# Kernel tuning notes

Hardware: AMD Instinct MI355X
Metric: run time of the kernel (lower is better)

Reference implementation:

```python
import jax, jax.numpy as jnp
import numpy as np

N = 20000       # nodes
E = 320000      # edges (before self-loops)
F_IN = 1024     # num_features
H = 4           # head_num
C = 64          # hidden_size
NC = 4          # n_classes
NEG_SLOPE = 0.2 # PyG GATConv default


def setup_inputs() -> dict:
    key = jax.random.key(0)
    ks = jax.random.split(key, 16)
    def w(k, shape, fan_in):
        return jax.random.normal(k, shape, dtype=jnp.float32) / np.sqrt(fan_in)
    x = jax.random.normal(ks[0], (N, F_IN), dtype=jnp.float32)
    edge_index = jax.random.randint(ks[1], (2, E), 0, N, dtype=jnp.int64)
    return {
        "x": x,
        "edge_index": edge_index,
        # layer 1: F_IN -> H*C, concat
        "w1": w(ks[2], (F_IN, H * C), F_IN),
        "as1": w(ks[3], (H, C), C),
        "ad1": w(ks[4], (H, C), C),
        "b1": jnp.zeros((H * C,), jnp.float32),
        # layer 2: H*C -> H*C, concat
        "w2": w(ks[5], (H * C, H * C), H * C),
        "as2": w(ks[6], (H, C), C),
        "ad2": w(ks[7], (H, C), C),
        "b2": jnp.zeros((H * C,), jnp.float32),
        # out layer: H*C -> C, 1 head, concat=False
        "w3": w(ks[8], (H * C, 1 * C), H * C),
        "as3": w(ks[9], (1, C), C),
        "ad3": w(ks[10], (1, C), C),
        "b3": jnp.zeros((C,), jnp.float32),
        # classifier
        "wc": w(ks[11], (C, NC), C),
        "bc": jnp.zeros((NC,), jnp.float32),
    }


def gat_layer(x, src, dst, W, a_src, a_dst, bias, concat):
    """PyG GATConv (eval mode, self-loops already added to src/dst)."""
    n = x.shape[0]
    Hh, Cc = a_src.shape
    h = (x @ W).reshape(n, Hh, Cc)                       # [N,H,C]
    al_s = jnp.sum(h * a_src[None], axis=-1)             # [N,H]
    al_d = jnp.sum(h * a_dst[None], axis=-1)             # [N,H]
    e = al_s[src] + al_d[dst]                            # [E,H]
    e = jax.nn.leaky_relu(e, NEG_SLOPE)
    # segment softmax over incoming edges of each destination node
    emax = jax.ops.segment_max(e, dst, num_segments=n)   # [N,H]
    ex = jnp.exp(e - emax[dst])
    denom = jax.ops.segment_sum(ex, dst, num_segments=n) # [N,H]
    alpha = ex / (denom[dst] + 1e-16)                    # [E,H]
    msg = h[src] * alpha[..., None]                      # [E,H,C]
    out = jax.ops.segment_sum(msg, dst, num_segments=n)  # [N,H,C]
    if concat:
        out = out.reshape(n, Hh * Cc)
    else:
        out = out.mean(axis=1)
    return out + bias


def reference(x, edge_index, w1, as1, ad1, b1, w2, as2, ad2, b2,
              w3, as3, ad3, b3, wc, bc):
    n = x.shape[0]
    loop = jnp.arange(n, dtype=edge_index.dtype)
    src = jnp.concatenate([edge_index[0], loop])
    dst = jnp.concatenate([edge_index[1], loop])
    out = jax.nn.relu(gat_layer(x, src, dst, w1, as1, ad1, b1, True))
    out = jax.nn.relu(gat_layer(out, src, dst, w2, as2, ad2, b2, True))
    out = gat_layer(out, src, dst, w3, as3, ad3, b3, False)
    return out @ wc + bc                                  # [N, n_classes]
```

## Files before the change

### kernel.cpp

```cpp
#include <hip/hip_runtime.h>

#define N_NODES 20000
#define N_EDGES 320000
#define ET (N_EDGES + N_NODES)
#define F_IN 1024
#define HC 256
#define NC 4

typedef unsigned short ushort_t;
typedef __attribute__((ext_vector_type(8))) short short8;
typedef __attribute__((ext_vector_type(4))) float f32x4;

__device__ inline ushort_t f2bf(float f) {
    unsigned u = __float_as_uint(f);
    unsigned r = (u + 0x7fffu + ((u >> 16) & 1u)) >> 16;
    return (ushort_t)r;
}
__device__ inline float bf2f(ushort_t u) {
    return __uint_as_float(((unsigned)u) << 16);
}

__device__ inline unsigned cvt_pk_bf16(float lo, float hi) {
    unsigned r;
    asm("v_cvt_pk_bf16_f32 %0, %1, %2" : "=v"(r) : "v"(lo), "v"(hi));
    return r;
}

#define GLOAD16(gp, lp) __builtin_amdgcn_global_load_lds( \
    (const __attribute__((address_space(1))) void*)(gp),  \
    (__attribute__((address_space(3))) void*)(lp), 16, 0, 0)

__global__ void count_kernel(const int* __restrict__ ei, int* __restrict__ counts) {
    int e = blockIdx.x * blockDim.x + threadIdx.x;
    if (e >= ET) return;
    int dst = (e < N_EDGES) ? ei[N_EDGES + e] : (e - N_EDGES);
    atomicAdd(&counts[dst], 1);
}

__global__ void scan_kernel(const int* __restrict__ counts, int* __restrict__ row_ptr,
                            int* __restrict__ cursor) {
    __shared__ int sums[1024];
    int t = threadIdx.x;
    const int per = (N_NODES + 1023) / 1024;
    int b = t * per;
    int e = min(b + per, N_NODES);
    int s = 0;
    for (int i = b; i < e; ++i) s += counts[i];
    sums[t] = s;
    __syncthreads();
    for (int off = 1; off < 1024; off <<= 1) {
        int v = (t >= off) ? sums[t - off] : 0;
        __syncthreads();
        sums[t] += v;
        __syncthreads();
    }
    int run = (t == 0) ? 0 : sums[t - 1];
    for (int i = b; i < e; ++i) {
        row_ptr[i] = run;
        cursor[i]  = run;
        run += counts[i];
    }
    if (t == 0) row_ptr[N_NODES] = ET;
}

__global__ void scatter_kernel(const int* __restrict__ ei, int* __restrict__ cursor,
                               int* __restrict__ col) {
    int e = blockIdx.x * blockDim.x + threadIdx.x;
    if (e >= ET) return;
    int src, dst;
    if (e < N_EDGES) { src = ei[e]; dst = ei[N_EDGES + e]; }
    else             { src = dst = e - N_EDGES; }
    int pos = atomicAdd(&cursor[dst], 1);
    col[pos] = src;
}

__global__ void split_T(const float* __restrict__ in, ushort_t* __restrict__ hi,
                        ushort_t* __restrict__ lo, int K, int Nn) {
    int idx = blockIdx.x * blockDim.x + threadIdx.x;
    if (idx >= K * Nn) return;
    int k = idx / Nn, n = idx - k * Nn;
    float v = in[idx];
    ushort_t h = f2bf(v);
    hi[(size_t)n * K + k] = h;
    lo[(size_t)n * K + k] = f2bf(v - bf2f(h));
}

#define AL_EPILOGUE()                                                              \
    {                                                                              \
        float asv[NF], adv[NF];                                                    \
        _Pragma("unroll")                                                          \
        for (int j = 0; j < NF; ++j) {                                             \
            int col = bn + wn * SN + j * 16 + (lane & 15);                         \
            asv[j] = as_w[col];                                                    \
            adv[j] = ad_w[col];                                                    \
        }                                                                          \
        float* s_as = (float*)smem;                                   \
        float* s_ad = (float*)smem + 2 * BM;                                       \
        _Pragma("unroll")                                                          \
        for (int i = 0; i < MF; ++i) {                                             \
            _Pragma("unroll")                                                      \
            for (int rr = 0; rr < 4; ++rr) {                                       \
                float ps = 0.f, pd = 0.f;                                          \
                _Pragma("unroll")                                                  \
                for (int j = 0; j < NF; ++j) {                                     \
                    ps += acc[i][j][rr] * asv[j];                                  \
                    pd += acc[i][j][rr] * adv[j];                                  \
                }                                                                  \
                _Pragma("unroll")                                                  \
                for (int o = 1; o < 16; o <<= 1) {                                 \
                    ps += __shfl_xor(ps, o, 64);                                   \
                    pd += __shfl_xor(pd, o, 64);                                   \
                }                                                                  \
                if ((lane & 15) == 0) {                                            \
                    int rl = wm * SM + i * 16 + (lane >> 4) * 4 + rr;              \
                    s_as[wn * BM + rl] = ps;                                       \
                    s_ad[wn * BM + rl] = pd;                                       \
                }                                                                  \
            }                                                                      \
        }                                                                          \
        __syncthreads();                                                           \
        if (t < BM) {                                                              \
            int row = bm + t;                                                      \
            if (row < M) {                                                         \
                int hb = bn >> 6;                                                  \
                als[row * H + hb] = s_as[t] + s_as[BM + t];                        \
                ald[row * H + hb] = s_ad[t] + s_ad[BM + t];                        \
            }                                                                      \
        }                                                                          \
    }

template<int GY, int H>
__launch_bounds__(256)
__global__ void gemm_f32a(const float* __restrict__ X,
                          const ushort_t* __restrict__ BTh, const ushort_t* __restrict__ BTl,
                          float* __restrict__ C, const float* __restrict__ as_w,
                          const float* __restrict__ ad_w, float* __restrict__ als,
                          float* __restrict__ ald, int M, int K, int NT) {
    constexpr int BM = 128, BN = 64, SM = 64, SN = 32, MF = 4, NF = 2;
    __shared__ __align__(16) char smem[49152];

    const int t = threadIdx.x, lane = t & 63, w = t >> 6;
    const int wm = w >> 1, wn = w & 1;
    const int nwg = gridDim.x;
    const int id = blockIdx.x;
    const int q = nwg >> 3, r = nwg & 7;
    const int xcd = id & 7, idx = id >> 3;
    const int logical = (xcd < r ? xcd * (q + 1) : r * (q + 1) + (xcd - r) * q) + idx;
    const int bm = (logical / GY) * BM, bn = (logical % GY) * BN;

    const int achk = lane & 3;
    const float* xRow[2]; int aoff[2];
    #pragma unroll
    for (int qq = 0; qq < 2; ++qq) {
        int arow = (w * 2 + qq) * 16 + (lane >> 2);
        int grow = min(bm + arow, M - 1);
        xRow[qq] = X + (size_t)grow * K + achk * 8;
        aoff[qq] = arow * 64 + ((achk ^ ((arow >> 1) & 3)) * 16);
    }
    const int gchunk = ((lane & 3) ^ ((lane >> 3) & 3)) * 16;
    const int brow = w * 16 + (lane >> 2);
    const size_t gB = (size_t)(bn + brow) * K * 2 + gchunk;
    const int lB = w * 1024;

    const char* Bhb = (const char*)BTh;
    const char* Blb = (const char*)BTl;
    const int c16 = (lane >> 4);
    const int NTs = K / 64;

    f32x4 acc[MF][NF];
    #pragma unroll
    for (int i = 0; i < MF; ++i)
        #pragma unroll
        for (int j = 0; j < NF; ++j) acc[i][j] = (f32x4){0.f, 0.f, 0.f, 0.f};

    float4 cur0[2][2], cur1[2][2], nxt0[2][2], nxt1[2][2];
    #pragma unroll
    for (int qq = 0; qq < 2; ++qq)
        #pragma unroll
        for (int kc = 0; kc < 2; ++kc) {
            cur0[qq][kc] = *(const float4*)(xRow[qq] + kc * 32);
            cur1[qq][kc] = *(const float4*)(xRow[qq] + kc * 32 + 4);
        }

    for (int ts = 0; ts < NTs; ++ts) {
        size_t kb = (size_t)ts * 128;
        #pragma unroll
        for (int kc = 0; kc < 2; ++kc) {
            GLOAD16(Bhb + gB + kb + kc * 64, smem + 32768 + kc * 4096 + lB);
            GLOAD16(Blb + gB + kb + kc * 64, smem + 40960 + kc * 4096 + lB);
        }
        if (ts + 1 < NTs) {
            #pragma unroll
            for (int qq = 0; qq < 2; ++qq)
                #pragma unroll
                for (int kc = 0; kc < 2; ++kc) {
                    nxt0[qq][kc] = *(const float4*)(xRow[qq] + (ts + 1) * 64 + kc * 32);
                    nxt1[qq][kc] = *(const float4*)(xRow[qq] + (ts + 1) * 64 + kc * 32 + 4);
                }
        }
        #pragma unroll
        for (int qq = 0; qq < 2; ++qq)
            #pragma unroll
            for (int kc = 0; kc < 2; ++kc) {
                float vv[8] = {cur0[qq][kc].x, cur0[qq][kc].y, cur0[qq][kc].z, cur0[qq][kc].w,
                               cur1[qq][kc].x, cur1[qq][kc].y, cur1[qq][kc].z, cur1[qq][kc].w};
                unsigned hp[4], lp[4];
                #pragma unroll
                for (int j = 0; j < 4; ++j) {
                    unsigned h = cvt_pk_bf16(vv[2 * j], vv[2 * j + 1]);
                    float h0 = __uint_as_float(h << 16);
                    float h1 = __uint_as_float(h & 0xFFFF0000u);
                    hp[j] = h;
                    lp[j] = cvt_pk_bf16(vv[2 * j] - h0, vv[2 * j + 1] - h1);
                }
                *(uint4*)(smem + kc * 8192 + aoff[qq])         = make_uint4(hp[0], hp[1], hp[2], hp[3]);
                *(uint4*)(smem + 16384 + kc * 8192 + aoff[qq]) = make_uint4(lp[0], lp[1], lp[2], lp[3]);
            }
        __syncthreads();
        #pragma unroll
        for (int kc = 0; kc < 2; ++kc) {
            short8 afh[MF], afl[MF], bfh[NF], bfl[NF];
            #pragma unroll
            for (int i = 0; i < MF; ++i) {
                int row = wm * SM + i * 16 + (lane & 15);
                int off = row * 64 + ((c16 ^ ((row >> 1) & 3)) * 16);
                afh[i] = *(const short8*)(smem + kc * 8192 + off);
                afl[i] = *(const short8*)(smem + 16384 + kc * 8192 + off);
            }
            #pragma unroll
            for (int j = 0; j < NF; ++j) {
                int row = wn * SN + j * 16 + (lane & 15);
                int off = row * 64 + ((c16 ^ ((row >> 1) & 3)) * 16);
                bfh[j] = *(const short8*)(smem + 32768 + kc * 4096 + off);
                bfl[j] = *(const short8*)(smem + 40960 + kc * 4096 + off);
            }
            #pragma unroll
            for (int i = 0; i < MF; ++i)
                #pragma unroll
                for (int j = 0; j < NF; ++j) {
                    acc[i][j] = __builtin_amdgcn_mfma_f32_16x16x32_bf16(afh[i], bfh[j], acc[i][j], 0, 0, 0);
                    acc[i][j] = __builtin_amdgcn_mfma_f32_16x16x32_bf16(afh[i], bfl[j], acc[i][j], 0, 0, 0);
                    acc[i][j] = __builtin_amdgcn_mfma_f32_16x16x32_bf16(afl[i], bfh[j], acc[i][j], 0, 0, 0);
                }
        }
        __syncthreads();
        #pragma unroll
        for (int qq = 0; qq < 2; ++qq)
            #pragma unroll
            for (int kc = 0; kc < 2; ++kc) { cur0[qq][kc] = nxt0[qq][kc]; cur1[qq][kc] = nxt1[qq][kc]; }
    }
    #pragma unroll
    for (int i = 0; i < MF; ++i) {
        int rbase = bm + wm * SM + i * 16 + (lane >> 4) * 4;
        #pragma unroll
        for (int j = 0; j < NF; ++j) {
            int col = bn + wn * SN + j * 16 + (lane & 15);
            #pragma unroll
            for (int rr = 0; rr < 4; ++rr)
                if (rbase + rr < M) C[(size_t)(rbase + rr) * NT + col] = acc[i][j][rr];
        }
    }
    AL_EPILOGUE()
}

template<int BMT, int GY, int H>
__launch_bounds__(256)
__global__ void gemm_mfma(const ushort_t* __restrict__ Ah, const ushort_t* __restrict__ Al,
                          const ushort_t* __restrict__ BTh, const ushort_t* __restrict__ BTl,
                          float* __restrict__ C, const float* __restrict__ as_w,
                          const float* __restrict__ ad_w, float* __restrict__ als,
                          float* __restrict__ ald, int M, int K, int NT) {
    constexpr int BM = BMT, BN = 64, SM = BM / 2, SN = 32, MF = SM / 16, NF = 2;
    constexpr int AQ = BM / 64;
    constexpr int ASZ = BM * 64;
    __shared__ __align__(16) char smem[4 * ASZ + 16384];

    const int t = threadIdx.x, lane = t & 63, w = t >> 6;
    const int wm = w >> 1, wn = w & 1;
    const int nwg = gridDim.x;
    const int id = blockIdx.x;
    const int q = nwg >> 3, r = nwg & 7;
    const int xcd = id & 7, idx = id >> 3;
    const int logical = (xcd < r ? xcd * (q + 1) : r * (q + 1) + (xcd - r) * q) + idx;
    const int bm = (logical / GY) * BM, bn = (logical % GY) * BN;
    const int gchunk = ((lane & 3) ^ ((lane >> 3) & 3)) * 16;

    size_t gA[AQ]; int lA[AQ];
    #pragma unroll
    for (int qq = 0; qq < AQ; ++qq) {
        int inst = w * AQ + qq;
        int arow = inst * 16 + (lane >> 2);
        int grow = min(bm + arow, M - 1);
        gA[qq] = (size_t)grow * K * 2 + gchunk;
        lA[qq] = inst * 1024;
    }
    const int brow = w * 16 + (lane >> 2);
    const size_t gB = (size_t)(bn + brow) * K * 2 + gchunk;
    const int lB = w * 1024;

    const char* Ahb = (const char*)Ah;
    const char* Alb = (const char*)Al;
    const char* Bhb = (const char*)BTh;
    const char* Blb = (const char*)BTl;
    const int c16 = (lane >> 4);
    const int NTs = K / 64;

    f32x4 acc[MF][NF];
    #pragma unroll
    for (int i = 0; i < MF; ++i)
        #pragma unroll
        for (int j = 0; j < NF; ++j) acc[i][j] = (f32x4){0.f, 0.f, 0.f, 0.f};

    for (int ts = 0; ts < NTs; ++ts) {
        size_t kb = (size_t)ts * 128;
        #pragma unroll
        for (int kc = 0; kc < 2; ++kc) {
            #pragma unroll
            for (int qq = 0; qq < AQ; ++qq) {
                GLOAD16(Ahb + gA[qq] + kb + kc * 64, smem + kc * ASZ + lA[qq]);
                GLOAD16(Alb + gA[qq] + kb + kc * 64, smem + 2 * ASZ + kc * ASZ + lA[qq]);
            }
            GLOAD16(Bhb + gB + kb + kc * 64, smem + 4 * ASZ + kc * 4096 + lB);
            GLOAD16(Blb + gB + kb + kc * 64, smem + 4 * ASZ + 8192 + kc * 4096 + lB);
        }
        __syncthreads();
        #pragma unroll
        for (int kc = 0; kc < 2; ++kc) {
            short8 afh[MF], afl[MF], bfh[NF], bfl[NF];
            #pragma unroll
            for (int i = 0; i < MF; ++i) {
                int row = wm * SM + i * 16 + (lane & 15);
                int off = row * 64 + ((c16 ^ ((row >> 1) & 3)) * 16);
                afh[i] = *(const short8*)(smem + kc * ASZ + off);
                afl[i] = *(const short8*)(smem + 2 * ASZ + kc * ASZ + off);
            }
            #pragma unroll
            for (int j = 0; j < NF; ++j) {
                int row = wn * SN + j * 16 + (lane & 15);
                int off = row * 64 + ((c16 ^ ((row >> 1) & 3)) * 16);
                bfh[j] = *(const short8*)(smem + 4 * ASZ + kc * 4096 + off);
                bfl[j] = *(const short8*)(smem + 4 * ASZ + 8192 + kc * 4096 + off);
            }
            #pragma unroll
            for (int i = 0; i < MF; ++i)
                #pragma unroll
                for (int j = 0; j < NF; ++j) {
                    acc[i][j] = __builtin_amdgcn_mfma_f32_16x16x32_bf16(afh[i], bfh[j], acc[i][j], 0, 0, 0);
                    acc[i][j] = __builtin_amdgcn_mfma_f32_16x16x32_bf16(afh[i], bfl[j], acc[i][j], 0, 0, 0);
                    acc[i][j] = __builtin_amdgcn_mfma_f32_16x16x32_bf16(afl[i], bfh[j], acc[i][j], 0, 0, 0);
                }
        }
        __syncthreads();
    }
    #pragma unroll
    for (int i = 0; i < MF; ++i) {
        int rbase = bm + wm * SM + i * 16 + (lane >> 4) * 4;
        #pragma unroll
        for (int j = 0; j < NF; ++j) {
            int col = bn + wn * SN + j * 16 + (lane & 15);
            #pragma unroll
            for (int rr = 0; rr < 4; ++rr)
                if (rbase + rr < M) C[(size_t)(rbase + rr) * NT + col] = acc[i][j][rr];
        }
    }
    AL_EPILOGUE()
}

template<int H>
__launch_bounds__(256)
__global__ void alpha_kernel(const float* __restrict__ als, const float* __restrict__ ald,
                             const int* __restrict__ row_ptr, const int* __restrict__ col,
                             float* __restrict__ alpha) {
    int lane = threadIdx.x & 63, w = threadIdx.x >> 6;
    int dst = blockIdx.x * 4 + w;
    if (dst >= N_NODES) return;
    int beg = row_ptr[dst], deg = row_ptr[dst + 1] - beg;
    constexpr int ES = 64 / H;
    int i_loc = lane / H, hh = lane % H;
    float ad = ald[dst * H + hh];
    float m = -1e30f, den = 0.f;
    for (int base = 0; base < deg; base += ES) {
        int i = base + i_loc;
        if (i < deg) {
            float e = als[col[beg + i] * H + hh] + ad;
            e = (e > 0.f) ? e : 0.2f * e;
            float nm = fmaxf(m, e);
            den = den * __expf(m - nm) + __expf(e - nm);
            m = nm;
        }
    }
    #pragma unroll
    for (int off = H; off < 64; off <<= 1) {
        float mo = __shfl_xor(m, off, 64);
        float dn = __shfl_xor(den, off, 64);
        float nm = fmaxf(m, mo);
        den = den * __expf(m - nm) + dn * __expf(mo - nm);
        m = nm;
    }
    float rden = 1.f / (den + 1e-16f);
    for (int base = 0; base < deg; base += ES) {
        int i = base + i_loc;
        if (i < deg) {
            float e = als[col[beg + i] * H + hh] + ad;
            e = (e > 0.f) ? e : 0.2f * e;
            alpha[(size_t)hh * ET + beg + i] = __expf(e - m) * rden;
        }
    }
}

template<int CT, int CW, int H, bool RELU, bool SPLIT>
__launch_bounds__(256)
__global__ void agg_v3(const float* __restrict__ h, const float* __restrict__ alpha,
                       const int* __restrict__ row_ptr, const int* __restrict__ col,
                       const float* __restrict__ bias,
                       ushort_t* __restrict__ oh, ushort_t* __restrict__ ol,
                       float* __restrict__ of) {
    constexpr int NS  = CT / CW;
    constexpr int LPT = CW / 4;
    constexpr int TPW = 64 / LPT;
    static_assert(NS == H, "slice==head mapping");
    __shared__ int   s_src[4][64];
    __shared__ float s_alp[4][64];
    const int nwg = gridDim.x;
    const int q = nwg >> 3;
    int id = blockIdx.x;
    int logical = (id & 7) * q + (id >> 3);
    int slice = logical / (N_NODES / 4);
    int g = logical - slice * (N_NODES / 4);
    int lane = threadIdx.x & 63, w = threadIdx.x >> 6;
    int dst = g * 4 + w;
    int beg = row_ptr[dst], deg = row_ptr[dst + 1] - beg;
    int team = lane / LPT;
    int cc = (lane & (LPT - 1)) * 4;

    const int*   colP = col + beg;
    const float* aP   = alpha + (size_t)slice * ET + beg;
    const float* hS   = h + slice * CW + cc;

    float4 acc = make_float4(0.f, 0.f, 0.f, 0.f);
    for (int base = 0; base < deg; base += 64) {
        int cnt = min(64, deg - base);
        if (lane < cnt) {
            s_src[w][lane] = colP[base + lane];
            s_alp[w][lane] = aP[base + lane];
        }
        for (int i = team; i < cnt; i += TPW) {
            int   s = s_src[w][i];
            float a = s_alp[w][i];
            float4 hv = *(const float4*)&hS[s * CT];
            acc.x += a * hv.x; acc.y += a * hv.y;
            acc.z += a * hv.z; acc.w += a * hv.w;
        }
    }
    #pragma unroll
    for (int off = LPT; off < 64; off <<= 1) {
        acc.x += __shfl_xor(acc.x, off, 64);
        acc.y += __shfl_xor(acc.y, off, 64);
        acc.z += __shfl_xor(acc.z, off, 64);
        acc.w += __shfl_xor(acc.w, off, 64);
    }
    if (team == 0) {
        int ch = slice * CW + cc;
        float4 bv = *(const float4*)&bias[ch];
        float v0 = acc.x + bv.x, v1 = acc.y + bv.y, v2 = acc.z + bv.z, v3 = acc.w + bv.w;
        if (RELU) {
            v0 = fmaxf(v0, 0.f); v1 = fmaxf(v1, 0.f);
            v2 = fmaxf(v2, 0.f); v3 = fmaxf(v3, 0.f);
        }
        size_t idx = (size_t)dst * CT + ch;
        if (SPLIT) {
            ushort4 h4, l4;
            h4.x = f2bf(v0); l4.x = f2bf(v0 - bf2f(h4.x));
            h4.y = f2bf(v1); l4.y = f2bf(v1 - bf2f(h4.y));
            h4.z = f2bf(v2); l4.z = f2bf(v2 - bf2f(h4.z));
            h4.w = f2bf(v3); l4.w = f2bf(v3 - bf2f(h4.w));
            *(ushort4*)&oh[idx] = h4;
            *(ushort4*)&ol[idx] = l4;
        } else {
            *(float4*)&of[idx] = make_float4(v0, v1, v2, v3);
        }
    }
}

__global__ void classifier_kernel(const float* __restrict__ x, const float* __restrict__ wc,
                                  const float* __restrict__ bc, float* __restrict__ out) {
    int n = blockIdx.x * blockDim.x + threadIdx.x;
    if (n >= N_NODES) return;
    float acc[NC] = {bc[0], bc[1], bc[2], bc[3]};
    for (int c = 0; c < 64; ++c) {
        float xv = x[(size_t)n * 64 + c];
        #pragma unroll
        for (int k = 0; k < NC; ++k) acc[k] += xv * wc[c * NC + k];
    }
    #pragma unroll
    for (int k = 0; k < NC; ++k) out[(size_t)n * NC + k] = acc[k];
}

extern "C" void kernel_launch(void* const* d_in, const int* in_sizes, int n_in,
                              void* d_out, int out_size, void* d_ws, size_t ws_size,
                              hipStream_t stream) {
    const float* x   = (const float*)d_in[0];
    const int*   ei  = (const int*)d_in[1];
    const float* w1  = (const float*)d_in[2];
    const float* as1 = (const float*)d_in[3];
    const float* ad1 = (const float*)d_in[4];
    const float* b1  = (const float*)d_in[5];
    const float* w2  = (const float*)d_in[6];
    const float* as2 = (const float*)d_in[7];
    const float* ad2 = (const float*)d_in[8];
    const float* b2  = (const float*)d_in[9];
    const float* w3  = (const float*)d_in[10];
    const float* as3 = (const float*)d_in[11];
    const float* ad3 = (const float*)d_in[12];
    const float* b3  = (const float*)d_in[13];
    const float* wc  = (const float*)d_in[14];
    const float* bc  = (const float*)d_in[15];
    float* out = (float*)d_out;

    char* ws = (char*)d_ws;
    size_t off = 0;
    auto alloc = [&](size_t bytes) -> char* {
        char* p = ws + off;
        off = (off + bytes + 255) & ~(size_t)255;
        return p;
    };

    int* counts  = (int*)alloc(N_NODES * 4);
    int* cursor  = (int*)alloc(N_NODES * 4);
    int* row_ptr = (int*)alloc((N_NODES + 1) * 4);
    int* colidx  = (int*)alloc(ET * 4);
    float* als   = (float*)alloc(N_NODES * 4 * 4);
    float* ald   = (float*)alloc(N_NODES * 4 * 4);
    float* alpha = (float*)alloc((size_t)4 * ET * 4);
    float* B0    = (float*)alloc((size_t)N_NODES * HC * 4);

    ushort_t* w1Th = (ushort_t*)alloc((size_t)F_IN * HC * 2);
    ushort_t* w1Tl = (ushort_t*)alloc((size_t)F_IN * HC * 2);
    ushort_t* w2Th = (ushort_t*)alloc((size_t)HC * HC * 2);
    ushort_t* w2Tl = (ushort_t*)alloc((size_t)HC * HC * 2);
    ushort_t* w3Th = (ushort_t*)alloc((size_t)HC * 64 * 2);
    ushort_t* w3Tl = (ushort_t*)alloc((size_t)HC * 64 * 2);
    ushort_t* B1h  = (ushort_t*)alloc((size_t)N_NODES * HC * 2);
    ushort_t* B1l  = (ushort_t*)alloc((size_t)N_NODES * HC * 2);
    float*    B1f  = (float*)alloc((size_t)N_NODES * 64 * 4);

    hipMemsetAsync(counts, 0, N_NODES * sizeof(int), stream);
    int eb = (ET + 255) / 256;
    count_kernel<<<eb, 256, 0, stream>>>(ei, counts);
    scan_kernel<<<1, 1024, 0, stream>>>(counts, row_ptr, cursor);
    scatter_kernel<<<eb, 256, 0, stream>>>(ei, cursor, colidx);

    split_T<<<(F_IN * HC + 255) / 256, 256, 0, stream>>>(w1, w1Th, w1Tl, F_IN, HC);
    split_T<<<(HC * HC + 255) / 256, 256, 0, stream>>>(w2, w2Th, w2Tl, HC, HC);
    split_T<<<(HC * 64 + 255) / 256, 256, 0, stream>>>(w3, w3Th, w3Tl, HC, 64);

    const int nwg128 = ((N_NODES + 127) / 128) * (HC / 64);
    const int nblk_dst = N_NODES / 4;
    gemm_f32a<4, 4><<<nwg128, 256, 0, stream>>>(x, w1Th, w1Tl, B0, as1, ad1, als, ald,
                                                N_NODES, F_IN, HC);
    alpha_kernel<4><<<nblk_dst, 256, 0, stream>>>(als, ald, row_ptr, colidx, alpha);
    agg_v3<256, 64, 4, true, true><<<4 * nblk_dst, 256, 0, stream>>>(
        B0, alpha, row_ptr, colidx, b1, B1h, B1l, nullptr);
    gemm_mfma<128, 4, 4><<<nwg128, 256, 0, stream>>>(B1h, B1l, w2Th, w2Tl, B0, as2, ad2,
                                                     als, ald, N_NODES, HC, HC);
    alpha_kernel<4><<<nblk_dst, 256, 0, stream>>>(als, ald, row_ptr, colidx, alpha);
    agg_v3<256, 64, 4, true, true><<<4 * nblk_dst, 256, 0, stream>>>(
        B0, alpha, row_ptr, colidx, b2, B1h, B1l, nullptr);
    const int nwg3 = (N_NODES + 63) / 64;
    gemm_mfma<64, 1, 1><<<nwg3, 256, 0, stream>>>(B1h, B1l, w3Th, w3Tl, B0, as3, ad3,
                                                  als, ald, N_NODES, HC, 64);
    alpha_kernel<1><<<nblk_dst, 256, 0, stream>>>(als, ald, row_ptr, colidx, alpha);
    agg_v3<64, 64, 1, false, false><<<nblk_dst, 256, 0, stream>>>(
        B0, alpha, row_ptr, colidx, b3, nullptr, nullptr, B1f);
    classifier_kernel<<<(N_NODES + 255) / 256, 256, 0, stream>>>(B1f, wc, bc, out);
}
```

Baseline: 292.2 us.

## Split-K first GEMM, unroll aggregation gathers, fuse classifier into last aggregation

The first GEMM (K=1024) is split into two K-halves with twice as many workgroups, each writing a partial result. A new reduce kernel sums the partials and computes the attention logits. The aggregation loop is unrolled by two with separate accumulators so more gathers are in flight. The classifier is fused into the final aggregation's epilogue, which removes one kernel and an intermediate buffer. The split-K path adds an extra 20MB partial write and read plus one more launch in exchange for more parallelism in the GEMM.

After: 282.0 us. 1.04x faster.

```diff
diff --git a/kernel.cpp b/kernel.cpp
--- a/kernel.cpp
+++ b/kernel.cpp
@@ -129,13 +129,12 @@
         }                                                                          \
     }
 
-template<int GY, int H>
+template<int GY>
 __launch_bounds__(256)
-__global__ void gemm_f32a(const float* __restrict__ X,
-                          const ushort_t* __restrict__ BTh, const ushort_t* __restrict__ BTl,
-                          float* __restrict__ C, const float* __restrict__ as_w,
-                          const float* __restrict__ ad_w, float* __restrict__ als,
-                          float* __restrict__ ald, int M, int K, int NT) {
+__global__ void gemm_f32a_ks(const float* __restrict__ X,
+                             const ushort_t* __restrict__ BTh, const ushort_t* __restrict__ BTl,
+                             float* __restrict__ Cp0, float* __restrict__ Cp1,
+                             int M, int K, int NT) {
     constexpr int BM = 128, BN = 64, SM = 64, SN = 32, MF = 4, NF = 2;
     __shared__ __align__(16) char smem[49152];
 
@@ -146,7 +145,12 @@
     const int q = nwg >> 3, r = nwg & 7;
     const int xcd = id & 7, idx = id >> 3;
     const int logical = (xcd < r ? xcd * (q + 1) : r * (q + 1) + (xcd - r) * q) + idx;
-    const int bm = (logical / GY) * BM, bn = (logical % GY) * BN;
+    const int nwg_half = nwg >> 1;
+    const int ks = logical / nwg_half;
+    const int rem = logical - ks * nwg_half;
+    const int bm = (rem / GY) * BM, bn = (rem % GY) * BN;
+    const int kbase = ks * (K >> 1);
+    float* Cp = ks ? Cp1 : Cp0;
 
     const int achk = lane & 3;
     const float* xRow[2]; int aoff[2];
@@ -154,18 +158,18 @@
     for (int qq = 0; qq < 2; ++qq) {
         int arow = (w * 2 + qq) * 16 + (lane >> 2);
         int grow = min(bm + arow, M - 1);
-        xRow[qq] = X + (size_t)grow * K + achk * 8;
+        xRow[qq] = X + (size_t)grow * K + kbase + achk * 8;
         aoff[qq] = arow * 64 + ((achk ^ ((arow >> 1) & 3)) * 16);
     }
     const int gchunk = ((lane & 3) ^ ((lane >> 3) & 3)) * 16;
     const int brow = w * 16 + (lane >> 2);
-    const size_t gB = (size_t)(bn + brow) * K * 2 + gchunk;
+    const size_t gB = (size_t)(bn + brow) * K * 2 + (size_t)kbase * 2 + gchunk;
     const int lB = w * 1024;
 
     const char* Bhb = (const char*)BTh;
     const char* Blb = (const char*)BTl;
     const int c16 = (lane >> 4);
-    const int NTs = K / 64;
+    const int NTs = K >> 7;
 
     f32x4 acc[MF][NF];
     #pragma unroll
@@ -257,10 +261,38 @@
             int col = bn + wn * SN + j * 16 + (lane & 15);
             #pragma unroll
             for (int rr = 0; rr < 4; ++rr)
-                if (rbase + rr < M) C[(size_t)(rbase + rr) * NT + col] = acc[i][j][rr];
-        }
-    }
-    AL_EPILOGUE()
+                if (rbase + rr < M) Cp[(size_t)(rbase + rr) * NT + col] = acc[i][j][rr];
+        }
+    }
+}
+
+__launch_bounds__(256)
+__global__ void reduce_al(float* __restrict__ B0, const float* __restrict__ Cp1,
+                          const float* __restrict__ as_w, const float* __restrict__ ad_w,
+                          float* __restrict__ als, float* __restrict__ ald) {
+    int lane = threadIdx.x & 63, w = threadIdx.x >> 6;
+    int row = blockIdx.x * 4 + w;
+    if (row >= N_NODES) return;
+    size_t base = (size_t)row * HC + lane * 4;
+    float4 p0 = *(const float4*)&B0[base];
+    float4 p1 = *(const float4*)&Cp1[base];
+    float4 s = make_float4(p0.x + p1.x, p0.y + p1.y, p0.z + p1.z, p0.w + p1.w);
+    *(float4*)&B0[base] = s;
+    int head = lane >> 4;
+    int cw = (lane & 15) * 4;
+    float ps = s.x * as_w[head * 64 + cw + 0] + s.y * as_w[head * 64 + cw + 1]
+             + s.z * as_w[head * 64 + cw + 2] + s.w * as_w[head * 64 + cw + 3];
+    float pd = s.x * ad_w[head * 64 + cw + 0] + s.y * ad_w[head * 64 + cw + 1]
+             + s.z * ad_w[head * 64 + cw + 2] + s.w * ad_w[head * 64 + cw + 3];
+    #pragma unroll
+    for (int o = 1; o < 16; o <<= 1) {
+        ps += __shfl_xor(ps, o, 64);
+        pd += __shfl_xor(pd, o, 64);
+    }
+    if ((lane & 15) == 0) {
+        als[row * 4 + head] = ps;
+        ald[row * 4 + head] = pd;
+    }
 }
 
 template<int BMT, int GY, int H>
@@ -408,13 +440,15 @@
     }
 }
 
-template<int CT, int CW, int H, bool RELU, bool SPLIT>
+template<int CT, int CW, int H, bool RELU, bool SPLIT, bool CLS>
 __launch_bounds__(256)
-__global__ void agg_v3(const float* __restrict__ h, const float* __restrict__ alpha,
+__global__ void agg_v4(const float* __restrict__ h, const float* __restrict__ alpha,
                        const int* __restrict__ row_ptr, const int* __restrict__ col,
                        const float* __restrict__ bias,
                        ushort_t* __restrict__ oh, ushort_t* __restrict__ ol,
-                       float* __restrict__ of) {
+                       float* __restrict__ of,
+                       const float* __restrict__ wc, const float* __restrict__ bc,
+                       float* __restrict__ cls_out) {
     constexpr int NS  = CT / CW;
     constexpr int LPT = CW / 4;
     constexpr int TPW = 64 / LPT;
@@ -437,21 +471,31 @@
     const float* aP   = alpha + (size_t)slice * ET + beg;
     const float* hS   = h + slice * CW + cc;
 
-    float4 acc = make_float4(0.f, 0.f, 0.f, 0.f);
+    float4 acc  = make_float4(0.f, 0.f, 0.f, 0.f);
+    float4 acc2 = make_float4(0.f, 0.f, 0.f, 0.f);
     for (int base = 0; base < deg; base += 64) {
         int cnt = min(64, deg - base);
         if (lane < cnt) {
             s_src[w][lane] = colP[base + lane];
             s_alp[w][lane] = aP[base + lane];
         }
-        for (int i = team; i < cnt; i += TPW) {
-            int   s = s_src[w][i];
-            float a = s_alp[w][i];
-            float4 hv = *(const float4*)&hS[s * CT];
-            acc.x += a * hv.x; acc.y += a * hv.y;
-            acc.z += a * hv.z; acc.w += a * hv.w;
-        }
-    }
+        int i = team;
+        for (; i + TPW < cnt; i += 2 * TPW) {
+            int   s0 = s_src[w][i],       s1 = s_src[w][i + TPW];
+            float a0 = s_alp[w][i],       a1 = s_alp[w][i + TPW];
+            float4 h0 = *(const float4*)&hS[s0 * CT];
+            float4 h1 = *(const float4*)&hS[s1 * CT];
+            acc.x  += a0 * h0.x; acc.y  += a0 * h0.y; acc.z  += a0 * h0.z; acc.w  += a0 * h0.w;
+            acc2.x += a1 * h1.x; acc2.y += a1 * h1.y; acc2.z += a1 * h1.z; acc2.w += a1 * h1.w;
+        }
+        if (i < cnt) {
+            int   s0 = s_src[w][i];
+            float a0 = s_alp[w][i];
+            float4 h0 = *(const float4*)&hS[s0 * CT];
+            acc.x += a0 * h0.x; acc.y += a0 * h0.y; acc.z += a0 * h0.z; acc.w += a0 * h0.w;
+        }
+    }
+    acc.x += acc2.x; acc.y += acc2.y; acc.z += acc2.z; acc.w += acc2.w;
     #pragma unroll
     for (int off = LPT; off < 64; off <<= 1) {
         acc.x += __shfl_xor(acc.x, off, 64);
@@ -467,33 +511,35 @@
             v0 = fmaxf(v0, 0.f); v1 = fmaxf(v1, 0.f);
             v2 = fmaxf(v2, 0.f); v3 = fmaxf(v3, 0.f);
         }
-        size_t idx = (size_t)dst * CT + ch;
-        if (SPLIT) {
-            ushort4 h4, l4;
-            h4.x = f2bf(v0); l4.x = f2bf(v0 - bf2f(h4.x));
-            h4.y = f2bf(v1); l4.y = f2bf(v1 - bf2f(h4.y));
-            h4.z = f2bf(v2); l4.z = f2bf(v2 - bf2f(h4.z));
-            h4.w = f2bf(v3); l4.w = f2bf(v3 - bf2f(h4.w));
-            *(ushort4*)&oh[idx] = h4;
-            *(ushort4*)&ol[idx] = l4;
+        if (CLS) {
+            float ps[NC];
+            #pragma unroll
+            for (int k = 0; k < NC; ++k)
+                ps[k] = v0 * wc[(cc + 0) * NC + k] + v1 * wc[(cc + 1) * NC + k]
+                      + v2 * wc[(cc + 2) * NC + k] + v3 * wc[(cc + 3) * NC + k];
+            #pragma unroll
+            for (int o = 1; o < 16; o <<= 1)
+                #pragma unroll
+                for (int k = 0; k < NC; ++k) ps[k] += __shfl_xor(ps[k], o, 64);
+            if (lane == 0) {
+                #pragma unroll
+                for (int k = 0; k < NC; ++k) cls_out[(size_t)dst * NC + k] = ps[k] + bc[k];
+            }
         } else {
-            *(float4*)&of[idx] = make_float4(v0, v1, v2, v3);
-        }
-    }
-}
-
-__global__ void classifier_kernel(const float* __restrict__ x, const float* __restrict__ wc,
-                                  const float* __restrict__ bc, float* __restrict__ out) {
-    int n = blockIdx.x * blockDim.x + threadIdx.x;
-    if (n >= N_NODES) return;
-    float acc[NC] = {bc[0], bc[1], bc[2], bc[3]};
-    for (int c = 0; c < 64; ++c) {
-        float xv = x[(size_t)n * 64 + c];
-        #pragma unroll
-        for (int k = 0; k < NC; ++k) acc[k] += xv * wc[c * NC + k];
-    }
-    #pragma unroll
-    for (int k = 0; k < NC; ++k) out[(size_t)n * NC + k] = acc[k];
+            size_t idx = (size_t)dst * CT + ch;
+            if (SPLIT) {
+                ushort4 h4, l4;
+                h4.x = f2bf(v0); l4.x = f2bf(v0 - bf2f(h4.x));
+                h4.y = f2bf(v1); l4.y = f2bf(v1 - bf2f(h4.y));
+                h4.z = f2bf(v2); l4.z = f2bf(v2 - bf2f(h4.z));
+                h4.w = f2bf(v3); l4.w = f2bf(v3 - bf2f(h4.w));
+                *(ushort4*)&oh[idx] = h4;
+                *(ushort4*)&ol[idx] = l4;
+            } else {
+                *(float4*)&of[idx] = make_float4(v0, v1, v2, v3);
+            }
+        }
+    }
 }
 
 extern "C" void kernel_launch(void* const* d_in, const int* in_sizes, int n_in,
@@ -533,6 +579,7 @@
     float* ald   = (float*)alloc(N_NODES * 4 * 4);
     float* alpha = (float*)alloc((size_t)4 * ET * 4);
     float* B0    = (float*)alloc((size_t)N_NODES * HC * 4);
+    float* Cp1   = (float*)alloc((size_t)N_NODES * HC * 4);
 
     ushort_t* w1Th = (ushort_t*)alloc((size_t)F_IN * HC * 2);
     ushort_t* w1Tl = (ushort_t*)alloc((size_t)F_IN * HC * 2);
@@ -542,7 +589,6 @@
     ushort_t* w3Tl = (ushort_t*)alloc((size_t)HC * 64 * 2);
     ushort_t* B1h  = (ushort_t*)alloc((size_t)N_NODES * HC * 2);
     ushort_t* B1l  = (ushort_t*)alloc((size_t)N_NODES * HC * 2);
-    float*    B1f  = (float*)alloc((size_t)N_NODES * 64 * 4);
 
     hipMemsetAsync(counts, 0, N_NODES * sizeof(int), stream);
     int eb = (ET + 255) / 256;
@@ -556,21 +602,20 @@
 
     const int nwg128 = ((N_NODES + 127) / 128) * (HC / 64);
     const int nblk_dst = N_NODES / 4;
-    gemm_f32a<4, 4><<<nwg128, 256, 0, stream>>>(x, w1Th, w1Tl, B0, as1, ad1, als, ald,
-                                                N_NODES, F_IN, HC);
+    gemm_f32a_ks<4><<<2 * nwg128, 256, 0, stream>>>(x, w1Th, w1Tl, B0, Cp1, N_NODES, F_IN, HC);
+    reduce_al<<<nblk_dst, 256, 0, stream>>>(B0, Cp1, as1, ad1, als, ald);
     alpha_kernel<4><<<nblk_dst, 256, 0, stream>>>(als, ald, row_ptr, colidx, alpha);
-    agg_v3<256, 64, 4, true, true><<<4 * nblk_dst, 256, 0, stream>>>(
-        B0, alpha, row_ptr, colidx, b1, B1h, B1l, nullptr);
+    agg_v4<256, 64, 4, true, true, false><<<4 * nblk_dst, 256, 0, stream>>>(
+        B0, alpha, row_ptr, colidx, b1, B1h, B1l, nullptr, nullptr, nullptr, nullptr);
     gemm_mfma<128, 4, 4><<<nwg128, 256, 0, stream>>>(B1h, B1l, w2Th, w2Tl, B0, as2, ad2,
                                                      als, ald, N_NODES, HC, HC);
     alpha_kernel<4><<<nblk_dst, 256, 0, stream>>>(als, ald, row_ptr, colidx, alpha);
-    agg_v3<256, 64, 4, true, true><<<4 * nblk_dst, 256, 0, stream>>>(
-        B0, alpha, row_ptr, colidx, b2, B1h, B1l, nullptr);
+    agg_v4<256, 64, 4, true, true, false><<<4 * nblk_dst, 256, 0, stream>>>(
+        B0, alpha, row_ptr, colidx, b2, B1h, B1l, nullptr, nullptr, nullptr, nullptr);
     const int nwg3 = (N_NODES + 63) / 64;
     gemm_mfma<64, 1, 1><<<nwg3, 256, 0, stream>>>(B1h, B1l, w3Th, w3Tl, B0, as3, ad3,
                                                   als, ald, N_NODES, HC, 64);
     alpha_kernel<1><<<nblk_dst, 256, 0, stream>>>(als, ald, row_ptr, colidx, alpha);
-    agg_v3<64, 64, 1, false, false><<<nblk_dst, 256, 0, stream>>>(
-        B0, alpha, row_ptr, colidx, b3, nullptr, nullptr, B1f);
-    classifier_kernel<<<(N_NODES + 255) / 256, 256, 0, stream>>>(B1f, wc, bc, out);
-}
+    agg_v4<64, 64, 1, false, false, true><<<nblk_dst, 256, 0, stream>>>(
+        B0, alpha, row_ptr, colidx, b3, nullptr, nullptr, nullptr, wc, bc, out);
+}
```
